# Kernel optimization log

Measured on AMD Instinct MI355X. Metric: run time of the kernel, lower is better.

## Reference

```python
import jax, jax.numpy as jnp
import numpy as np

V, E, H, F, B = 32000, 1024, 1024, 2048, 64
NL = 8  # number of GRU cells


def _gru_cell(x, h, Wih, Whh, bih, bhh):
    # PyTorch GRU single-step math. x:[B,E], h:[B,H], Wih:[3H,E], Whh:[3H,H]
    gi = x @ Wih.T + bih            # [B,3H]
    gh = h @ Whh.T + bhh            # [B,3H]
    i_r, i_z, i_n = jnp.split(gi, 3, axis=1)
    h_r, h_z, h_n = jnp.split(gh, 3, axis=1)
    r = jax.nn.sigmoid(i_r + h_r)
    z = jax.nn.sigmoid(i_z + h_z)
    n = jnp.tanh(i_n + r * h_n)
    return (1.0 - z) * n + z * h


def setup_inputs() -> dict:
    key = jax.random.key(0)
    ks = jax.random.split(key, 20)
    s = 0.02
    inp = {
        "feature": jax.random.normal(ks[0], (B, F), jnp.float32),
        "x": jax.random.randint(ks[1], (B,), 0, V),
        "attention": jax.random.normal(ks[2], (B, H), jnp.float32),
        "hiddens": jax.random.normal(ks[3], (NL, B, H), jnp.float32),
        "emb": jax.random.normal(ks[4], (V, E), jnp.float32) * s,
        "map_W": jax.random.normal(ks[5], (H, F), jnp.float32) * s,
        "map_b": jnp.zeros((H,), jnp.float32),
        "ai_W": jax.random.normal(ks[6], (H, H), jnp.float32) * s,
        "ai_b": jnp.zeros((H,), jnp.float32),
        "ah_W": jax.random.normal(ks[7], (H, H), jnp.float32) * s,
        "ah_b": jnp.zeros((H,), jnp.float32),
        "ao_W": jax.random.normal(ks[8], (H, H), jnp.float32) * s,
        "ao_b": jnp.zeros((H,), jnp.float32),
        "gru_Wih": jax.random.normal(ks[9], (NL, 3 * H, E), jnp.float32) * s,
        "gru_Whh": jax.random.normal(ks[10], (NL, 3 * H, H), jnp.float32) * s,
        "gru_bih": jnp.zeros((NL, 3 * H), jnp.float32),
        "gru_bhh": jnp.zeros((NL, 3 * H), jnp.float32),
        "out_W": jax.random.normal(ks[11], (V, H), jnp.float32) * s,
        "out_b": jnp.zeros((V,), jnp.float32),
    }
    return inp


def reference(feature, x, attention, hiddens, emb, map_W, map_b, ai_W, ai_b,
              ah_W, ah_b, ao_W, ao_b, gru_Wih, gru_Whh, gru_bih, gru_bhh,
              out_W, out_b):
    xe = jax.nn.relu(emb[x])                                  # [B,E]
    feat = jax.nn.relu(feature @ map_W.T + map_b)             # [B,H]
    attn = jax.nn.relu((feat + attention) @ ai_W.T + ai_b)
    attn = jax.nn.relu(attn @ ah_W.T + ah_b)
    attn = jax.nn.relu(attn @ ao_W.T + ao_b)                  # [B,H]

    def cell(i, xin):
        return _gru_cell(xin, hiddens[i] + attn, gru_Wih[i], gru_Whh[i],
                         gru_bih[i], gru_bhh[i])

    h1 = cell(0, xe)          # new attention output
    x2 = cell(1, h1)
    x3 = cell(2, x2)
    x4 = cell(3, x2 + x3)
    x5 = cell(4, x3 + x4)
    x6 = cell(5, x4 + x5)
    x7 = cell(6, x5 + x6)
    x8 = cell(7, x6 + x7)

    logp = jax.nn.log_softmax(x8 @ out_W.T + out_b, axis=1)   # [B,V]
    new_hiddens = jnp.stack([h1, x2, x3, x4, x5, x6, x7, x8])  # [8,B,H]
    return (logp, h1, new_hiddens)
```

## Files before the change

kernel.cpp:

```cpp
#include <hip/hip_runtime.h>
#include <math.h>

typedef __bf16 bf16x8 __attribute__((ext_vector_type(8)));
typedef __bf16 bf16x4 __attribute__((ext_vector_type(4)));
typedef float f32x4 __attribute__((ext_vector_type(4)));

__device__ __forceinline__ void atomAdd(float* p, float v) {
#if __has_builtin(__builtin_amdgcn_global_atomic_fadd_f32)
    unsafeAtomicAdd(p, v);
#else
    atomicAdd(p, v);
#endif
}

__device__ __forceinline__ bf16x8 cvt8(const float* p) {
    f32x4 lo = *reinterpret_cast<const f32x4*>(p);
    f32x4 hi = *reinterpret_cast<const f32x4*>(p + 4);
    bf16x8 r;
#pragma unroll
    for (int i = 0; i < 4; ++i) { r[i] = (__bf16)lo[i]; r[i + 4] = (__bf16)hi[i]; }
    return r;
}

__global__ __launch_bounds__(256) void gemm_acc(
    const __bf16* __restrict__ A, long long Asb,
    const float* __restrict__ W, long long Wsb,
    float* __restrict__ out, long long osb,
    int K, int KC, int N)
{
    const int l = threadIdx.x & 63;
    const int wave = threadIdx.x >> 6;
    const int lane16 = l & 15;
    const int quad = l >> 4;
    const int layer = blockIdx.z;
    const int n = (blockIdx.x * 4 + wave) * 16 + lane16;
    const int k0 = blockIdx.y * KC;

    A += (long long)layer * Asb + k0 + quad * 8;
    const float* wp = W + (long long)layer * Wsb + (long long)n * K + k0 + quad * 8;
    const __bf16* ap0 = A + (long long)(lane16 +  0) * K;
    const __bf16* ap1 = A + (long long)(lane16 + 16) * K;
    const __bf16* ap2 = A + (long long)(lane16 + 32) * K;
    const __bf16* ap3 = A + (long long)(lane16 + 48) * K;

    f32x4 acc0 = {0.f, 0.f, 0.f, 0.f};
    f32x4 acc1 = acc0, acc2 = acc0, acc3 = acc0;

#pragma unroll 4
    for (int k = 0; k < KC; k += 32) {
        bf16x8 b  = cvt8(wp + k);
        bf16x8 a0 = *reinterpret_cast<const bf16x8*>(ap0 + k);
        bf16x8 a1 = *reinterpret_cast<const bf16x8*>(ap1 + k);
        bf16x8 a2 = *reinterpret_cast<const bf16x8*>(ap2 + k);
        bf16x8 a3 = *reinterpret_cast<const bf16x8*>(ap3 + k);
        acc0 = __builtin_amdgcn_mfma_f32_16x16x32_bf16(a0, b, acc0, 0, 0, 0);
        acc1 = __builtin_amdgcn_mfma_f32_16x16x32_bf16(a1, b, acc1, 0, 0, 0);
        acc2 = __builtin_amdgcn_mfma_f32_16x16x32_bf16(a2, b, acc2, 0, 0, 0);
        acc3 = __builtin_amdgcn_mfma_f32_16x16x32_bf16(a3, b, acc3, 0, 0, 0);
    }

    f32x4 accs[4] = {acc0, acc1, acc2, acc3};
    float* ob = out + (long long)layer * osb + n;
#pragma unroll
    for (int mt = 0; mt < 4; ++mt)
#pragma unroll
        for (int r = 0; r < 4; ++r) {
            const int m = mt * 16 + quad * 4 + r;
            atomAdd(ob + (long long)m * N, accs[mt][r]);
        }
}

template <int RELU, int RES>
__global__ __launch_bounds__(256) void conv_bf(
    const float* __restrict__ in, const float* __restrict__ res,
    __bf16* __restrict__ out, int total4)
{
    const int gid = blockIdx.x * 256 + threadIdx.x;
    if (gid >= total4) return;
    f32x4 v = reinterpret_cast<const f32x4*>(in)[gid];
    f32x4 rv;
    if (RES) rv = reinterpret_cast<const f32x4*>(res)[gid];
    bf16x4 o;
#pragma unroll
    for (int i = 0; i < 4; ++i) {
        float a = v[i];
        if (RELU) a = fmaxf(a, 0.0f);
        if (RES) a += rv[i];
        o[i] = (__bf16)a;
    }
    reinterpret_cast<bf16x4*>(out)[gid] = o;
}

__global__ __launch_bounds__(256) void init_acc(
    const float* __restrict__ map_b,
    const float* __restrict__ ai_b, const float* __restrict__ ah_b,
    const float* __restrict__ ao_b, const float* __restrict__ gru_bhh,
    const float* __restrict__ gru_bih, const float* __restrict__ out_b,
    float* __restrict__ t0, float* __restrict__ a1b, float* __restrict__ a2b,
    float* __restrict__ attnb, float* __restrict__ gh, float* __restrict__ gi,
    float* __restrict__ logp)
{
    int idx = blockIdx.x * 256 + threadIdx.x;
    if (idx < 65536) { t0[idx] = map_b[idx & 1023]; return; }
    idx -= 65536;
    if (idx < 65536) { a1b[idx] = ai_b[idx & 1023]; return; }
    idx -= 65536;
    if (idx < 65536) { a2b[idx] = ah_b[idx & 1023]; return; }
    idx -= 65536;
    if (idx < 65536) { attnb[idx] = ao_b[idx & 1023]; return; }
    idx -= 65536;
    if (idx < 1572864) {
        const int layer = idx / 196608, col = idx % 3072;
        gh[idx] = gru_bhh[layer * 3072 + col];
        return;
    }
    idx -= 1572864;
    if (idx < 1572864) {
        const int layer = idx / 196608, col = idx % 3072;
        gi[idx] = gru_bih[layer * 3072 + col];
        return;
    }
    idx -= 1572864;
    if (idx < 2048000) logp[idx] = out_b[idx % 32000];
}

__global__ __launch_bounds__(256) void gather_relu(
    const float* __restrict__ emb, const int* __restrict__ xidx,
    __bf16* __restrict__ xe)
{
    const int gid = blockIdx.x * 256 + threadIdx.x;
    const int m = gid >> 8, e = (gid & 255) << 2;
    f32x4 v = *reinterpret_cast<const f32x4*>(emb + (long long)xidx[m] * 1024 + e);
    bf16x4 o;
#pragma unroll
    for (int i = 0; i < 4; ++i) o[i] = (__bf16)fmaxf(v[i], 0.0f);
    *reinterpret_cast<bf16x4*>(xe + ((long long)m << 10) + e) = o;
}

__global__ __launch_bounds__(256) void hsum(
    const float* __restrict__ hiddens, const float* __restrict__ attn,
    __bf16* __restrict__ hbf)
{
    const int gid = blockIdx.x * 256 + threadIdx.x;
    f32x4 hv = reinterpret_cast<const f32x4*>(hiddens)[gid];
    f32x4 av = reinterpret_cast<const f32x4*>(attn)[gid & 16383];
    bf16x4 o;
#pragma unroll
    for (int i = 0; i < 4; ++i) o[i] = (__bf16)(hv[i] + fmaxf(av[i], 0.0f));
    reinterpret_cast<bf16x4*>(hbf)[gid] = o;
}

__global__ __launch_bounds__(256) void gru_pw(
    const float* __restrict__ gi, const float* __restrict__ gh,
    const float* __restrict__ hiddens, const float* __restrict__ attn,
    const float* __restrict__ oprev,
    float* __restrict__ o_out, float* __restrict__ o_out2,
    __bf16* __restrict__ xin_next)
{
    const int gid = blockIdx.x * 256 + threadIdx.x;
    const int m = gid >> 10, nn = gid & 1023;
    const long long gb = (long long)m * 3072 + nn;
    const float i_r = gi[gb], i_z = gi[gb + 1024], i_n = gi[gb + 2048];
    const float h_r = gh[gb], h_z = gh[gb + 1024], h_n = gh[gb + 2048];
    const float r = 1.0f / (1.0f + __expf(-(i_r + h_r)));
    const float z = 1.0f / (1.0f + __expf(-(i_z + h_z)));
    const float nv = tanhf(i_n + r * h_n);
    const float hcur = hiddens[gid] + fmaxf(attn[gid], 0.0f);
    const float x = (1.0f - z) * nv + z * hcur;
    o_out[gid] = x;
    if (o_out2) o_out2[gid] = x;
    float xi = x;
    if (oprev) xi += oprev[gid];
    xin_next[gid] = (__bf16)xi;
}

__global__ __launch_bounds__(256) void rowstats(
    const float* __restrict__ logits, float* __restrict__ stats)
{
    const int m = blockIdx.x;
    const f32x4* row = reinterpret_cast<const f32x4*>(logits + (long long)m * 32000);
    __shared__ float red[256];
    const int tid = threadIdx.x;
    float mx = -1e30f;
    for (int i = tid; i < 8000; i += 256) {
        f32x4 v = row[i];
        mx = fmaxf(mx, fmaxf(fmaxf(v[0], v[1]), fmaxf(v[2], v[3])));
    }
    red[tid] = mx;
    __syncthreads();
    for (int off = 128; off > 0; off >>= 1) {
        if (tid < off) red[tid] = fmaxf(red[tid], red[tid + off]);
        __syncthreads();
    }
    mx = red[0];
    __syncthreads();
    float s = 0.0f;
    for (int i = tid; i < 8000; i += 256) {
        f32x4 v = row[i];
        s += __expf(v[0] - mx) + __expf(v[1] - mx) + __expf(v[2] - mx) + __expf(v[3] - mx);
    }
    red[tid] = s;
    __syncthreads();
    for (int off = 128; off > 0; off >>= 1) {
        if (tid < off) red[tid] += red[tid + off];
        __syncthreads();
    }
    if (tid == 0) stats[m] = mx + logf(red[0]);
}

__global__ __launch_bounds__(256) void logp_k(
    float* __restrict__ out, const float* __restrict__ stats)
{
    const int n = blockIdx.x * 256 + threadIdx.x;
    const int m = blockIdx.y;
    const long long idx = (long long)m * 32000 + n;
    out[idx] = out[idx] - stats[m];
}

extern "C" void kernel_launch(void* const* d_in, const int* in_sizes, int n_in,
                              void* d_out, int out_size, void* d_ws, size_t ws_size,
                              hipStream_t stream)
{
    const float* feature   = (const float*)d_in[0];
    const int*   x         = (const int*)d_in[1];
    const float* attention = (const float*)d_in[2];
    const float* hiddens   = (const float*)d_in[3];
    const float* emb       = (const float*)d_in[4];
    const float* map_W     = (const float*)d_in[5];
    const float* map_b     = (const float*)d_in[6];
    const float* ai_W      = (const float*)d_in[7];
    const float* ai_b      = (const float*)d_in[8];
    const float* ah_W      = (const float*)d_in[9];
    const float* ah_b      = (const float*)d_in[10];
    const float* ao_W      = (const float*)d_in[11];
    const float* ao_b      = (const float*)d_in[12];
    const float* gru_Wih   = (const float*)d_in[13];
    const float* gru_Whh   = (const float*)d_in[14];
    const float* gru_bih   = (const float*)d_in[15];
    const float* gru_bhh   = (const float*)d_in[16];
    const float* out_W     = (const float*)d_in[17];
    const float* out_b     = (const float*)d_in[18];

    float* out      = (float*)d_out;
    float* out_logp = out;
    float* out_h1   = out + 2048000;
    float* out_nh   = out + 2048000 + 65536;

    float* w = (float*)d_ws;
    float* t0    = w + 0;
    float* a1b   = w + 65536;
    float* a2b   = w + 131072;
    float* attnb = w + 196608;
    float* gh    = w + 262144;
    float* gi    = w + 1835008;
    float* stats = w + 3407872;
    __bf16* xin   = (__bf16*)(w + 3407936);
    __bf16* featb = (__bf16*)(w + 3440704);
    __bf16* a1A   = (__bf16*)(w + 3506240);
    __bf16* a2A   = (__bf16*)(w + 3539008);
    __bf16* a3A   = (__bf16*)(w + 3571776);
    __bf16* hbf   = (__bf16*)(w + 3604544);

    init_acc<<<21312, 256, 0, stream>>>(map_b, ai_b, ah_b, ao_b,
                                        gru_bhh, gru_bih, out_b,
                                        t0, a1b, a2b, attnb, gh, gi, out_logp);
    gather_relu<<<64, 256, 0, stream>>>(emb, x, xin);
    conv_bf<0, 0><<<128, 256, 0, stream>>>(feature, nullptr, featb, 32768);

    gemm_acc<<<dim3(16, 16, 1), 256, 0, stream>>>(featb, 0, map_W, 0,
                                                  t0, 0, 2048, 128, 1024);
    conv_bf<1, 1><<<64, 256, 0, stream>>>(t0, attention, a1A, 16384);
    gemm_acc<<<dim3(16, 8, 1), 256, 0, stream>>>(a1A, 0, ai_W, 0,
                                                 a1b, 0, 1024, 128, 1024);
    conv_bf<1, 0><<<64, 256, 0, stream>>>(a1b, nullptr, a2A, 16384);
    gemm_acc<<<dim3(16, 8, 1), 256, 0, stream>>>(a2A, 0, ah_W, 0,
                                                 a2b, 0, 1024, 128, 1024);
    conv_bf<1, 0><<<64, 256, 0, stream>>>(a2b, nullptr, a3A, 16384);
    gemm_acc<<<dim3(16, 8, 1), 256, 0, stream>>>(a3A, 0, ao_W, 0,
                                                 attnb, 0, 1024, 128, 1024);

    hsum<<<512, 256, 0, stream>>>(hiddens, attnb, hbf);

    gemm_acc<<<dim3(48, 2, 8), 256, 0, stream>>>(hbf, 65536, gru_Whh, 3145728,
                                                 gh, 196608, 1024, 512, 3072);

    for (int c = 0; c < 8; ++c) {
        gemm_acc<<<dim3(48, 8, 1), 256, 0, stream>>>(
            xin, 0, gru_Wih + (long long)c * 3145728, 0,
            gi + (long long)c * 196608, 0, 1024, 128, 3072);
        gru_pw<<<256, 256, 0, stream>>>(
            gi + (long long)c * 196608, gh + (long long)c * 196608,
            hiddens + (long long)c * 65536, attnb,
            (c >= 2 && c < 7) ? out_nh + (long long)(c - 1) * 65536 : nullptr,
            out_nh + (long long)c * 65536,
            (c == 0) ? out_h1 : nullptr,
            xin);
    }

    gemm_acc<<<dim3(500, 2, 1), 256, 0, stream>>>(xin, 0, out_W, 0,
                                                  out_logp, 0, 1024, 512, 32000);

    rowstats<<<64, 256, 0, stream>>>(out_logp, stats);
    logp_k<<<dim3(125, 64), 256, 0, stream>>>(out_logp, stats);
}
```

Before: 596.1 us.

## Drop split-K atomics, fuse bias/activation epilogues and GRU gates into GEMMs

Removes the bias-init pass and split-K atomic accumulation. Every GEMM now runs the full K loop per block and writes its result directly with the bias added. The attention MLP GEMMs fold ReLU, residual and bf16 conversion into their epilogue. Each GRU step computes the input projection and the gate math in one kernel, using ping-pong xin buffers. Row stats and the log-softmax subtraction are merged into one kernel. This cuts launches and atomic traffic, but each GEMM now has far fewer blocks (64 for the small ones, 48x8 for gh), so less of the GPU is kept busy during the sequential chain.

```diff
diff --git a/kernel.cpp b/kernel.cpp
--- a/kernel.cpp
+++ b/kernel.cpp
@@ -4,14 +4,6 @@
 typedef __bf16 bf16x8 __attribute__((ext_vector_type(8)));
 typedef __bf16 bf16x4 __attribute__((ext_vector_type(4)));
 typedef float f32x4 __attribute__((ext_vector_type(4)));
-
-__device__ __forceinline__ void atomAdd(float* p, float v) {
-#if __has_builtin(__builtin_amdgcn_global_atomic_fadd_f32)
-    unsafeAtomicAdd(p, v);
-#else
-    atomicAdd(p, v);
-#endif
-}
 
 __device__ __forceinline__ bf16x8 cvt8(const float* p) {
     f32x4 lo = *reinterpret_cast<const f32x4*>(p);
@@ -22,11 +14,16 @@
     return r;
 }
 
-__global__ __launch_bounds__(256) void gemm_acc(
+__device__ __forceinline__ float sigm(float v) {
+    return 1.0f / (1.0f + __expf(-v));
+}
+
+__global__ __launch_bounds__(256) void gemm_ns(
     const __bf16* __restrict__ A, long long Asb,
     const float* __restrict__ W, long long Wsb,
+    const float* __restrict__ bias, long long bsb,
     float* __restrict__ out, long long osb,
-    int K, int KC, int N)
+    int K, int N)
 {
     const int l = threadIdx.x & 63;
     const int wave = threadIdx.x >> 6;
@@ -34,10 +31,9 @@
     const int quad = l >> 4;
     const int layer = blockIdx.z;
     const int n = (blockIdx.x * 4 + wave) * 16 + lane16;
-    const int k0 = blockIdx.y * KC;
-
-    A += (long long)layer * Asb + k0 + quad * 8;
-    const float* wp = W + (long long)layer * Wsb + (long long)n * K + k0 + quad * 8;
+
+    A += (long long)layer * Asb + quad * 8;
+    const float* wp = W + (long long)layer * Wsb + (long long)n * K + quad * 8;
     const __bf16* ap0 = A + (long long)(lane16 +  0) * K;
     const __bf16* ap1 = A + (long long)(lane16 + 16) * K;
     const __bf16* ap2 = A + (long long)(lane16 + 32) * K;
@@ -47,7 +43,7 @@
     f32x4 acc1 = acc0, acc2 = acc0, acc3 = acc0;
 
 #pragma unroll 4
-    for (int k = 0; k < KC; k += 32) {
+    for (int k = 0; k < K; k += 32) {
         bf16x8 b  = cvt8(wp + k);
         bf16x8 a0 = *reinterpret_cast<const bf16x8*>(ap0 + k);
         bf16x8 a1 = *reinterpret_cast<const bf16x8*>(ap1 + k);
@@ -59,6 +55,7 @@
         acc3 = __builtin_amdgcn_mfma_f32_16x16x32_bf16(a3, b, acc3, 0, 0, 0);
     }
 
+    const float bv = bias[(long long)layer * bsb + n];
     f32x4 accs[4] = {acc0, acc1, acc2, acc3};
     float* ob = out + (long long)layer * osb + n;
 #pragma unroll
@@ -66,62 +63,114 @@
 #pragma unroll
         for (int r = 0; r < 4; ++r) {
             const int m = mt * 16 + quad * 4 + r;
-            atomAdd(ob + (long long)m * N, accs[mt][r]);
+            ob[(long long)m * N] = accs[mt][r] + bv;
         }
 }
 
-template <int RELU, int RES>
+template <int EPI>
+__global__ __launch_bounds__(256) void gemm_small(
+    const __bf16* __restrict__ A, const float* __restrict__ W,
+    const float* __restrict__ bias, const float* __restrict__ att,
+    __bf16* __restrict__ obf, float* __restrict__ of32, int K)
+{
+    const int l = threadIdx.x & 63;
+    const int wave = threadIdx.x >> 6;
+    const int lane16 = l & 15;
+    const int quad = l >> 4;
+    const int c = blockIdx.x * 16 + lane16;
+
+    const float* wp = W + (long long)c * K + quad * 8;
+    const __bf16* ap = A + (long long)(wave * 16 + lane16) * K + quad * 8;
+
+    f32x4 acc = {0.f, 0.f, 0.f, 0.f};
+#pragma unroll 8
+    for (int k = 0; k < K; k += 32) {
+        bf16x8 b = cvt8(wp + k);
+        bf16x8 a = *reinterpret_cast<const bf16x8*>(ap + k);
+        acc = __builtin_amdgcn_mfma_f32_16x16x32_bf16(a, b, acc, 0, 0, 0);
+    }
+
+    const float bv = bias[c];
+#pragma unroll
+    for (int r = 0; r < 4; ++r) {
+        const int m = wave * 16 + quad * 4 + r;
+        float v = acc[r] + bv;
+        if (EPI <= 1) {
+            v = fmaxf(v, 0.0f);
+            if (EPI == 1) v += att[m * 1024 + c];
+            obf[m * 1024 + c] = (__bf16)v;
+        } else {
+            of32[m * 1024 + c] = v;
+        }
+    }
+}
+
+__global__ __launch_bounds__(256) void gru_layer(
+    const __bf16* __restrict__ xin, const float* __restrict__ Wih,
+    const float* __restrict__ ghl, const float* __restrict__ hid_l,
+    const float* __restrict__ attnb, const float* __restrict__ bih,
+    const float* __restrict__ oprev,
+    float* __restrict__ o_out, float* __restrict__ o_h1,
+    __bf16* __restrict__ xnext)
+{
+    const int l = threadIdx.x & 63;
+    const int wave = threadIdx.x >> 6;
+    const int lane16 = l & 15;
+    const int quad = l >> 4;
+    const int c = blockIdx.x * 16 + lane16;
+
+    const __bf16* ap = xin + (long long)(wave * 16 + lane16) * 1024 + quad * 8;
+    const float* wp0 = Wih + (long long)(c       ) * 1024 + quad * 8;
+    const float* wp1 = Wih + (long long)(c + 1024) * 1024 + quad * 8;
+    const float* wp2 = Wih + (long long)(c + 2048) * 1024 + quad * 8;
+
+    f32x4 acc0 = {0.f, 0.f, 0.f, 0.f};
+    f32x4 acc1 = acc0, acc2 = acc0;
+
+#pragma unroll 4
+    for (int k = 0; k < 1024; k += 32) {
+        bf16x8 a  = *reinterpret_cast<const bf16x8*>(ap + k);
+        bf16x8 b0 = cvt8(wp0 + k);
+        bf16x8 b1 = cvt8(wp1 + k);
+        bf16x8 b2 = cvt8(wp2 + k);
+        acc0 = __builtin_amdgcn_mfma_f32_16x16x32_bf16(a, b0, acc0, 0, 0, 0);
+        acc1 = __builtin_amdgcn_mfma_f32_16x16x32_bf16(a, b1, acc1, 0, 0, 0);
+        acc2 = __builtin_amdgcn_mfma_f32_16x16x32_bf16(a, b2, acc2, 0, 0, 0);
+    }
+
+    const float b_r = bih[c], b_z = bih[c + 1024], b_n = bih[c + 2048];
+#pragma unroll
+    for (int r = 0; r < 4; ++r) {
+        const int m = wave * 16 + quad * 4 + r;
+        const float i_r = acc0[r] + b_r;
+        const float i_z = acc1[r] + b_z;
+        const float i_n = acc2[r] + b_n;
+        const float h_r = ghl[m * 3072 + c];
+        const float h_z = ghl[m * 3072 + c + 1024];
+        const float h_n = ghl[m * 3072 + c + 2048];
+        const float rr = sigm(i_r + h_r);
+        const float z  = sigm(i_z + h_z);
+        const float nv = tanhf(i_n + rr * h_n);
+        const float hcur = hid_l[m * 1024 + c] + fmaxf(attnb[m * 1024 + c], 0.0f);
+        const float x = (1.0f - z) * nv + z * hcur;
+        o_out[m * 1024 + c] = x;
+        if (o_h1) o_h1[m * 1024 + c] = x;
+        float xi = x;
+        if (oprev) xi += oprev[m * 1024 + c];
+        xnext[m * 1024 + c] = (__bf16)xi;
+    }
+}
+
 __global__ __launch_bounds__(256) void conv_bf(
-    const float* __restrict__ in, const float* __restrict__ res,
-    __bf16* __restrict__ out, int total4)
+    const float* __restrict__ in, __bf16* __restrict__ out, int total4)
 {
     const int gid = blockIdx.x * 256 + threadIdx.x;
     if (gid >= total4) return;
     f32x4 v = reinterpret_cast<const f32x4*>(in)[gid];
-    f32x4 rv;
-    if (RES) rv = reinterpret_cast<const f32x4*>(res)[gid];
     bf16x4 o;
 #pragma unroll
-    for (int i = 0; i < 4; ++i) {
-        float a = v[i];
-        if (RELU) a = fmaxf(a, 0.0f);
-        if (RES) a += rv[i];
-        o[i] = (__bf16)a;
-    }
+    for (int i = 0; i < 4; ++i) o[i] = (__bf16)v[i];
     reinterpret_cast<bf16x4*>(out)[gid] = o;
-}
-
-__global__ __launch_bounds__(256) void init_acc(
-    const float* __restrict__ map_b,
-    const float* __restrict__ ai_b, const float* __restrict__ ah_b,
-    const float* __restrict__ ao_b, const float* __restrict__ gru_bhh,
-    const float* __restrict__ gru_bih, const float* __restrict__ out_b,
-    float* __restrict__ t0, float* __restrict__ a1b, float* __restrict__ a2b,
-    float* __restrict__ attnb, float* __restrict__ gh, float* __restrict__ gi,
-    float* __restrict__ logp)
-{
-    int idx = blockIdx.x * 256 + threadIdx.x;
-    if (idx < 65536) { t0[idx] = map_b[idx & 1023]; return; }
-    idx -= 65536;
-    if (idx < 65536) { a1b[idx] = ai_b[idx & 1023]; return; }
-    idx -= 65536;
-    if (idx < 65536) { a2b[idx] = ah_b[idx & 1023]; return; }
-    idx -= 65536;
-    if (idx < 65536) { attnb[idx] = ao_b[idx & 1023]; return; }
-    idx -= 65536;
-    if (idx < 1572864) {
-        const int layer = idx / 196608, col = idx % 3072;
-        gh[idx] = gru_bhh[layer * 3072 + col];
-        return;
-    }
-    idx -= 1572864;
-    if (idx < 1572864) {
-        const int layer = idx / 196608, col = idx % 3072;
-        gi[idx] = gru_bih[layer * 3072 + col];
-        return;
-    }
-    idx -= 1572864;
-    if (idx < 2048000) logp[idx] = out_b[idx % 32000];
 }
 
 __global__ __launch_bounds__(256) void gather_relu(
@@ -150,35 +199,10 @@
     reinterpret_cast<bf16x4*>(hbf)[gid] = o;
 }
 
-__global__ __launch_bounds__(256) void gru_pw(
-    const float* __restrict__ gi, const float* __restrict__ gh,
-    const float* __restrict__ hiddens, const float* __restrict__ attn,
-    const float* __restrict__ oprev,
-    float* __restrict__ o_out, float* __restrict__ o_out2,
-    __bf16* __restrict__ xin_next)
-{
-    const int gid = blockIdx.x * 256 + threadIdx.x;
-    const int m = gid >> 10, nn = gid & 1023;
-    const long long gb = (long long)m * 3072 + nn;
-    const float i_r = gi[gb], i_z = gi[gb + 1024], i_n = gi[gb + 2048];
-    const float h_r = gh[gb], h_z = gh[gb + 1024], h_n = gh[gb + 2048];
-    const float r = 1.0f / (1.0f + __expf(-(i_r + h_r)));
-    const float z = 1.0f / (1.0f + __expf(-(i_z + h_z)));
-    const float nv = tanhf(i_n + r * h_n);
-    const float hcur = hiddens[gid] + fmaxf(attn[gid], 0.0f);
-    const float x = (1.0f - z) * nv + z * hcur;
-    o_out[gid] = x;
-    if (o_out2) o_out2[gid] = x;
-    float xi = x;
-    if (oprev) xi += oprev[gid];
-    xin_next[gid] = (__bf16)xi;
-}
-
-__global__ __launch_bounds__(256) void rowstats(
-    const float* __restrict__ logits, float* __restrict__ stats)
+__global__ __launch_bounds__(256) void softmax_k(float* __restrict__ logits)
 {
     const int m = blockIdx.x;
-    const f32x4* row = reinterpret_cast<const f32x4*>(logits + (long long)m * 32000);
+    f32x4* row = reinterpret_cast<f32x4*>(logits + (long long)m * 32000);
     __shared__ float red[256];
     const int tid = threadIdx.x;
     float mx = -1e30f;
@@ -205,16 +229,13 @@
         if (tid < off) red[tid] += red[tid + off];
         __syncthreads();
     }
-    if (tid == 0) stats[m] = mx + logf(red[0]);
-}
-
-__global__ __launch_bounds__(256) void logp_k(
-    float* __restrict__ out, const float* __restrict__ stats)
-{
-    const int n = blockIdx.x * 256 + threadIdx.x;
-    const int m = blockIdx.y;
-    const long long idx = (long long)m * 32000 + n;
-    out[idx] = out[idx] - stats[m];
+    const float lse = mx + logf(red[0]);
+    __syncthreads();
+    for (int i = tid; i < 8000; i += 256) {
+        f32x4 v = row[i];
+        v[0] -= lse; v[1] -= lse; v[2] -= lse; v[3] -= lse;
+        row[i] = v;
+    }
 }
 
 extern "C" void kernel_launch(void* const* d_in, const int* in_sizes, int n_in,
@@ -247,59 +268,50 @@
     float* out_nh   = out + 2048000 + 65536;
 
     float* w = (float*)d_ws;
-    float* t0    = w + 0;
-    float* a1b   = w + 65536;
-    float* a2b   = w + 131072;
-    float* attnb = w + 196608;
-    float* gh    = w + 262144;
-    float* gi    = w + 1835008;
-    float* stats = w + 3407872;
-    __bf16* xin   = (__bf16*)(w + 3407936);
-    __bf16* featb = (__bf16*)(w + 3440704);
-    __bf16* a1A   = (__bf16*)(w + 3506240);
-    __bf16* a2A   = (__bf16*)(w + 3539008);
-    __bf16* a3A   = (__bf16*)(w + 3571776);
-    __bf16* hbf   = (__bf16*)(w + 3604544);
-
-    init_acc<<<21312, 256, 0, stream>>>(map_b, ai_b, ah_b, ao_b,
-                                        gru_bhh, gru_bih, out_b,
-                                        t0, a1b, a2b, attnb, gh, gi, out_logp);
-    gather_relu<<<64, 256, 0, stream>>>(emb, x, xin);
-    conv_bf<0, 0><<<128, 256, 0, stream>>>(feature, nullptr, featb, 32768);
-
-    gemm_acc<<<dim3(16, 16, 1), 256, 0, stream>>>(featb, 0, map_W, 0,
-                                                  t0, 0, 2048, 128, 1024);
-    conv_bf<1, 1><<<64, 256, 0, stream>>>(t0, attention, a1A, 16384);
-    gemm_acc<<<dim3(16, 8, 1), 256, 0, stream>>>(a1A, 0, ai_W, 0,
-                                                 a1b, 0, 1024, 128, 1024);
-    conv_bf<1, 0><<<64, 256, 0, stream>>>(a1b, nullptr, a2A, 16384);
-    gemm_acc<<<dim3(16, 8, 1), 256, 0, stream>>>(a2A, 0, ah_W, 0,
-                                                 a2b, 0, 1024, 128, 1024);
-    conv_bf<1, 0><<<64, 256, 0, stream>>>(a2b, nullptr, a3A, 16384);
-    gemm_acc<<<dim3(16, 8, 1), 256, 0, stream>>>(a3A, 0, ao_W, 0,
-                                                 attnb, 0, 1024, 128, 1024);
+    float*  attnb = w + 0;
+    float*  gh    = w + 65536;
+    __bf16* featb = (__bf16*)(w + 1638400);
+    __bf16* a1A   = (__bf16*)(w + 1703936);
+    __bf16* a2A   = (__bf16*)(w + 1736704);
+    __bf16* a3A   = (__bf16*)(w + 1769472);
+    __bf16* xinA  = (__bf16*)(w + 1802240);
+    __bf16* xinB  = (__bf16*)(w + 1835008);
+    __bf16* hbf   = (__bf16*)(w + 1867776);
+    __bf16* xbuf[2] = {xinA, xinB};
+
+    gather_relu<<<64, 256, 0, stream>>>(emb, x, xinA);
+    conv_bf<<<128, 256, 0, stream>>>(feature, featb, 32768);
+
+    gemm_small<1><<<64, 256, 0, stream>>>(featb, map_W, map_b, attention,
+                                          a1A, nullptr, 2048);
+    gemm_small<0><<<64, 256, 0, stream>>>(a1A, ai_W, ai_b, nullptr,
+                                          a2A, nullptr, 1024);
+    gemm_small<0><<<64, 256, 0, stream>>>(a2A, ah_W, ah_b, nullptr,
+                                          a3A, nullptr, 1024);
+    gemm_small<2><<<64, 256, 0, stream>>>(a3A, ao_W, ao_b, nullptr,
+                                          nullptr, attnb, 1024);
 
     hsum<<<512, 256, 0, stream>>>(hiddens, attnb, hbf);
 
-    gemm_acc<<<dim3(48, 2, 8), 256, 0, stream>>>(hbf, 65536, gru_Whh, 3145728,
-                                                 gh, 196608, 1024, 512, 3072);
+    gemm_ns<<<dim3(48, 1, 8), 256, 0, stream>>>(hbf, 65536, gru_Whh, 3145728,
+                                                gru_bhh, 3072, gh, 196608,
+                                                1024, 3072);
 
     for (int c = 0; c < 8; ++c) {
-        gemm_acc<<<dim3(48, 8, 1), 256, 0, stream>>>(
-            xin, 0, gru_Wih + (long long)c * 3145728, 0,
-            gi + (long long)c * 196608, 0, 1024, 128, 3072);
-        gru_pw<<<256, 256, 0, stream>>>(
-            gi + (long long)c * 196608, gh + (long long)c * 196608,
+        gru_layer<<<64, 256, 0, stream>>>(
+            xbuf[c & 1], gru_Wih + (long long)c * 3145728,
+            gh + (long long)c * 196608,
             hiddens + (long long)c * 65536, attnb,
+            gru_bih + (long long)c * 3072,
             (c >= 2 && c < 7) ? out_nh + (long long)(c - 1) * 65536 : nullptr,
             out_nh + (long long)c * 65536,
             (c == 0) ? out_h1 : nullptr,
-            xin);
-    }
-
-    gemm_acc<<<dim3(500, 2, 1), 256, 0, stream>>>(xin, 0, out_W, 0,
-                                                  out_logp, 0, 1024, 512, 32000);
-
-    rowstats<<<64, 256, 0, stream>>>(out_logp, stats);
-    logp_k<<<dim3(125, 64), 256, 0, stream>>>(out_logp, stats);
-}
+            xbuf[(c + 1) & 1]);
+    }
+
+    gemm_ns<<<dim3(500, 1, 1), 256, 0, stream>>>(xbuf[0], 0, out_W, 0,
+                                                 out_b, 0, out_logp, 0,
+                                                 1024, 32000);
+
+    softmax_k<<<64, 256, 0, stream>>>(out_logp);
+}
```

Result: slower. 784.0 us (+31.5%).
